# Kernel optimization log

Hardware: AMD Instinct MI355X
Metric: run time of the kernel (lower is better)

The kernel has to match this reference:

```python
import jax, jax.numpy as jnp
import numpy as np

N_NODES = 50000
N_EDGES = 800000
DIM = 128
NUM_GRAPHS = 512


def setup_inputs() -> dict:
    key = jax.random.key(0)
    ks = jax.random.split(key, 12)
    s = 1.0 / np.sqrt(DIM)
    inp = {
        'x': jax.random.normal(ks[0], (N_NODES, DIM), dtype=jnp.float32),
        'edge_index': jax.random.randint(ks[1], (2, N_EDGES), 0, N_NODES, dtype=jnp.int32),
        'batch': jnp.sort(jax.random.randint(ks[2], (N_NODES,), 0, NUM_GRAPHS, dtype=jnp.int32)),
        'W1a': jax.random.uniform(ks[3], (DIM, DIM), jnp.float32, -s, s),
        'b1a': jax.random.uniform(ks[4], (DIM,), jnp.float32, -s, s),
        'W1b': jax.random.uniform(ks[5], (DIM, DIM), jnp.float32, -s, s),
        'b1b': jax.random.uniform(ks[6], (DIM,), jnp.float32, -s, s),
        'W2a': jax.random.uniform(ks[7], (DIM, DIM), jnp.float32, -s, s),
        'b2a': jax.random.uniform(ks[8], (DIM,), jnp.float32, -s, s),
        'W2b': jax.random.uniform(ks[9], (DIM, DIM), jnp.float32, -s, s),
        'b2b': jax.random.uniform(ks[10], (DIM,), jnp.float32, -s, s),
    }
    return inp


def _gin_conv(x, edge_index, Wa, ba, Wb, bb):
    # GINConv with eps=0: h_i = MLP(x_i + sum_{j->i} x_j)
    src, dst = edge_index[0], edge_index[1]
    agg = jax.ops.segment_sum(x[src], dst, num_segments=x.shape[0])  # [N, F]
    h = x + agg
    h = jax.nn.relu(h @ Wa + ba)
    return h @ Wb + bb


def reference(x, edge_index, batch, W1a, b1a, W1b, b1b, W2a, b2a, W2b, b2b):
    h = _gin_conv(x, edge_index, W1a, b1a, W1b, b1b)
    h = _gin_conv(h, edge_index, W2a, b2a, W2b, b2b)
    # global mean pool over graphs
    sums = jax.ops.segment_sum(h, batch, num_segments=NUM_GRAPHS)      # [G, F]
    counts = jax.ops.segment_sum(jnp.ones((h.shape[0],), h.dtype), batch, num_segments=NUM_GRAPHS)
    return sums / jnp.maximum(counts, 1.0)[:, None]
```

## Files before the change

kernel.cpp:

```cpp
#include <hip/hip_runtime.h>

#define DIM 128
#define NBUCK 784
#define EPB 8192
#define ELDS_CAP 2048

typedef unsigned short ushortT;
typedef unsigned int uintT;
typedef _Float16 f16;
typedef __attribute__((ext_vector_type(2))) _Float16 f16x2;
typedef __attribute__((ext_vector_type(8))) _Float16 f16x8;
typedef __attribute__((ext_vector_type(4))) float f32x4;

__device__ inline ushortT f2h(float f) { return __builtin_bit_cast(ushortT, (f16)f); }
__device__ inline float h2f(ushortT s) { return (float)__builtin_bit_cast(f16, s); }

__device__ inline int off_in_row(int k) {
    return (((k >> 5) * 4 + ((k & 15) >> 2)) << 4) + (((k >> 4) & 1) << 3) + ((k & 3) << 1);
}

__device__ inline void add4(f16x2* a, uint4 v) {
    a[0] += __builtin_bit_cast(f16x2, v.x);
    a[1] += __builtin_bit_cast(f16x2, v.y);
    a[2] += __builtin_bit_cast(f16x2, v.z);
    a[3] += __builtin_bit_cast(f16x2, v.w);
}

__device__ inline int wave_iscan(int v) {
    int lane = threadIdx.x & 63;
    #pragma unroll
    for (int d = 1; d < 64; d <<= 1) {
        int t = __shfl_up(v, d, 64);
        if (lane >= d) v += t;
    }
    return v;
}

__global__ __launch_bounds__(256)
void scan_blk_kernel(int* __restrict__ a, int n, int* __restrict__ bsum) {
    __shared__ int ws[4];
    const int tid = threadIdx.x;
    const int i = blockIdx.x * 256 + tid;
    const int lane = tid & 63, wv = tid >> 6;
    int v = (i < n) ? a[i] : 0;
    int isc = wave_iscan(v);
    if (lane == 63) ws[wv] = isc;
    __syncthreads();
    if (tid == 0) { int run = 0; for (int w = 0; w < 4; ++w) { int t = ws[w]; ws[w] = run; run += t; } }
    __syncthreads();
    int e = ws[wv] + isc - v;
    if (i < n) a[i] = e;
    if (tid == 255) bsum[blockIdx.x] = e + v;
}

__global__ __launch_bounds__(256)
void scan_add2_kernel(int* __restrict__ a, int n, const int* __restrict__ bsum) {
    __shared__ int ws[4];
    __shared__ int s_carry;
    const int tid = threadIdx.x;
    int partial = 0;
    for (int i = tid; i < (int)blockIdx.x; i += 256) partial += bsum[i];
    #pragma unroll
    for (int d = 1; d < 64; d <<= 1) partial += __shfl_xor(partial, d, 64);
    if ((tid & 63) == 0) ws[tid >> 6] = partial;
    __syncthreads();
    if (tid == 0) s_carry = ws[0] + ws[1] + ws[2] + ws[3];
    __syncthreads();
    int i = blockIdx.x * 256 + tid;
    if (i < n) a[i] += s_carry;
}

__global__ __launch_bounds__(256)
void histA_kernel(const int* __restrict__ dstIdx, int* __restrict__ histg, int ne, int nblk) {
    __shared__ int h[NBUCK];
    const int j = blockIdx.x;
    for (int i = threadIdx.x; i < NBUCK; i += 256) h[i] = 0;
    __syncthreads();
    const int base = j * EPB;
    const int end = (base + EPB < ne) ? base + EPB : ne;
    for (int i = base + threadIdx.x; i < end; i += 256)
        atomicAdd(&h[dstIdx[i] >> 6], 1);
    __syncthreads();
    for (int b = threadIdx.x; b < NBUCK; b += 256)
        histg[b * nblk + j] = h[b];
}

__global__ __launch_bounds__(256)
void fillA_kernel(const int* __restrict__ srcIdx, const int* __restrict__ dstIdx,
                  const int* __restrict__ Sg, uintT* __restrict__ pairs, int ne, int nblk) {
    __shared__ int cur[NBUCK];
    const int j = blockIdx.x;
    for (int i = threadIdx.x; i < NBUCK; i += 256) cur[i] = Sg[i * nblk + j];
    __syncthreads();
    const int base = j * EPB;
    const int end = (base + EPB < ne) ? base + EPB : ne;
    for (int i = base + threadIdx.x; i < end; i += 256) {
        const int d = dstIdx[i];
        const int s = srcIdx[i];
        const int b = d >> 6;
        const uintT E4 = ((uintT)s << 4) ^ (uintT)(s & 7);
        const int pos = atomicAdd(&cur[b], 1);
        pairs[pos] = (E4 << 6) | (uintT)(d & 63);
    }
}

__global__ __launch_bounds__(256)
void convert_prep_kernel(const float* __restrict__ x, ushortT* __restrict__ xb, int n,
                         const float* __restrict__ W0, const float* __restrict__ W1,
                         const float* __restrict__ W2, const float* __restrict__ W3,
                         ushortT* __restrict__ Wt) {
    if (blockIdx.x < 128) {
        int w = blockIdx.x >> 5;
        const float* W = (w == 0) ? W0 : (w == 1) ? W1 : (w == 2) ? W2 : W3;
        ushortT* dst = Wt + (size_t)w * DIM * DIM;
        int i = (blockIdx.x & 31) * 256 + threadIdx.x;
        int nidx = i >> 6, p = i & 63, k = 2 * p;
        float w0 = W[k * DIM + nidx];
        float w1 = W[(k + 1) * DIM + nidx];
        uintT u = ((uintT)f2h(w1) << 16) | f2h(w0);
        *(uintT*)((char*)dst + (size_t)nidx * 256 + (off_in_row(k) ^ ((nidx & 7) << 4))) = u;
        return;
    }
    int i = (blockIdx.x - 128) * 256 + threadIdx.x;
    int node = i >> 6, p = i & 63;
    if (node >= n) return;
    float2 v = *(const float2*)(x + (size_t)node * DIM + 2 * p);
    uintT u = ((uintT)f2h(v.y) << 16) | f2h(v.x);
    *(uintT*)((char*)xb + (size_t)node * 256 + (off_in_row(2 * p) ^ ((node & 7) << 4))) = u;
}

__global__ __launch_bounds__(128)
void graphoff_zero_kernel(const int* __restrict__ batch, int* __restrict__ goff,
                          float* __restrict__ out, int ng, int nn) {
    const int g = blockIdx.x;
    out[(size_t)g * DIM + threadIdx.x] = 0.0f;
    if (threadIdx.x == 0) {
        int lo = 0, hi = nn;
        while (lo < hi) { int mid = (lo + hi) >> 1; if (batch[mid] < g) lo = mid + 1; else hi = mid; }
        goff[g] = lo;
    }
}

template<int POOL>
__global__ __launch_bounds__(512, 4)
void fused_kernel(const ushortT* __restrict__ Xsrc, ushortT* __restrict__ Yg,
                  const uintT* __restrict__ pairs, const int* __restrict__ Sg, int nblk,
                  const ushortT* __restrict__ WtA, const float* __restrict__ ba,
                  const ushortT* __restrict__ WtB, const float* __restrict__ bb,
                  const int* __restrict__ batch, float* __restrict__ out, int n, int ne) {
    __shared__ __align__(16) ushortT XsU[64 * DIM];
    __shared__ int elds[ELDS_CAP];
    __shared__ int histc[64];
    __shared__ int lstart[65];
    __shared__ int bs[64];

    const int b = blockIdx.x;
    const int node0 = b * 64;
    const int tid = threadIdx.x;
    const int lane = tid & 63, wid = tid >> 6;

    const int base = Sg[b * nblk];
    const int endp = (b + 1 < NBUCK) ? Sg[(b + 1) * nblk] : ne;
    int cnt = endp - base;
    if (cnt > ELDS_CAP) cnt = ELDS_CAP;

    if (tid < 64) {
        histc[tid] = 0;
        if (POOL) { int node = node0 + tid; bs[tid] = (node < n) ? batch[node] : -1; }
    }
    __syncthreads();
    for (int i = tid; i < cnt; i += 512) atomicAdd(&histc[pairs[base + i] & 63], 1);
    __syncthreads();
    if (tid < 64) {
        int v = histc[tid];
        int isc = wave_iscan(v);
        lstart[tid] = isc - v;
        histc[tid] = isc - v;
        if (tid == 63) lstart[64] = isc;
    }
    __syncthreads();
    for (int i = tid; i < cnt; i += 512) {
        uintT p = pairs[base + i];
        int pos = atomicAdd(&histc[p & 63], 1);
        elds[pos] = (int)((p >> 6) << 4);
    }
    __syncthreads();

    const int l15 = lane & 15, g16 = lane >> 4;
    const int lofs = l15 << 4;
    const char* Xc = (const char*)Xsrc;
    for (int t = 0; t < 8; ++t) {
        const int r = wid * 8 + t;
        const int node = node0 + r;
        f16x2 a0[4], a1[4];
        #pragma unroll
        for (int j = 0; j < 4; ++j) { a0[j] = (f16x2)0; a1[j] = (f16x2)0; }
        if (node < n) {
            if (g16 == 0) {
                const int Es = (node << 8) ^ ((node & 7) << 4);
                add4(a0, *(const uint4*)(Xc + (Es ^ lofs)));
            }
            const int s0 = lstart[r], s1 = lstart[r + 1];
            int e = s0;
            for (; e + 16 <= s1; e += 16) {
                const int Ea = elds[e + g16];
                const int Eb = elds[e + 4 + g16];
                const int Ec = elds[e + 8 + g16];
                const int Ed = elds[e + 12 + g16];
                uint4 va = *(const uint4*)(Xc + (Ea ^ lofs));
                uint4 vb = *(const uint4*)(Xc + (Eb ^ lofs));
                uint4 vc = *(const uint4*)(Xc + (Ec ^ lofs));
                uint4 vd = *(const uint4*)(Xc + (Ed ^ lofs));
                add4(a0, va); add4(a1, vb); add4(a0, vc); add4(a1, vd);
            }
            for (; e + 4 <= s1; e += 4) {
                const int E = elds[e + g16];
                add4(a0, *(const uint4*)(Xc + (E ^ lofs)));
            }
            const int rem = s1 - e;
            if (g16 < rem) {
                const int E = elds[e + g16];
                add4(a1, *(const uint4*)(Xc + (E ^ lofs)));
            }
        }
        #pragma unroll
        for (int j = 0; j < 4; ++j) a0[j] += a1[j];
        #pragma unroll
        for (int j = 0; j < 4; ++j) {
            a0[j] += __builtin_bit_cast(f16x2, __shfl_xor(__builtin_bit_cast(int, a0[j]), 16));
            a0[j] += __builtin_bit_cast(f16x2, __shfl_xor(__builtin_bit_cast(int, a0[j]), 32));
        }
        if (lane < 16) {
            uint4 o;
            o.x = __builtin_bit_cast(uintT, a0[0]);
            o.y = __builtin_bit_cast(uintT, a0[1]);
            o.z = __builtin_bit_cast(uintT, a0[2]);
            o.w = __builtin_bit_cast(uintT, a0[3]);
            *(uint4*)((char*)XsU + ((r << 8) ^ (lofs ^ ((r & 7) << 4)))) = o;
        }
    }
    __syncthreads();

    const char* Xl = (const char*)XsU;
    const char* Wa = (const char*)WtA;
    const char* Wb = (const char*)WtB;
    const int g = lane >> 4;
    const int RB = (wid >> 2) * 32, CB = (wid & 3) * 32;

    f32x4 acc2[2][2];
    #pragma unroll
    for (int nt = 0; nt < 2; ++nt) {
        float bv = ba[CB + nt * 16 + l15];
        #pragma unroll
        for (int mt = 0; mt < 2; ++mt) acc2[mt][nt] = (f32x4){bv, bv, bv, bv};
    }
    #pragma unroll
    for (int ks = 0; ks < 4; ++ks) {
        const int cb = (ks * 4 + g) << 4;
        f16x8 a0, a1, bf[2];
        { int r0 = RB + l15, r1 = RB + 16 + l15;
          a0 = *(const f16x8*)(Xl + r0 * 256 + (cb ^ ((r0 & 7) << 4)));
          a1 = *(const f16x8*)(Xl + r1 * 256 + (cb ^ ((r1 & 7) << 4))); }
        #pragma unroll
        for (int nt = 0; nt < 2; ++nt) {
            int rn = CB + nt * 16 + l15;
            bf[nt] = *(const f16x8*)(Wa + rn * 256 + (cb ^ ((rn & 7) << 4)));
        }
        #pragma unroll
        for (int nt = 0; nt < 2; ++nt) {
            acc2[0][nt] = __builtin_amdgcn_mfma_f32_16x16x32_f16(a0, bf[nt], acc2[0][nt], 0, 0, 0);
            acc2[1][nt] = __builtin_amdgcn_mfma_f32_16x16x32_f16(a1, bf[nt], acc2[1][nt], 0, 0, 0);
        }
    }
    #pragma unroll
    for (int mt = 0; mt < 2; ++mt)
        #pragma unroll
        for (int nt = 0; nt < 2; ++nt)
            #pragma unroll
            for (int c = 0; c < 4; ++c) acc2[mt][nt][c] = fmaxf(acc2[mt][nt][c], 0.0f);

    __syncthreads();

    #pragma unroll
    for (int nt = 0; nt < 2; ++nt) {
        const int k = CB + nt * 16 + l15;
        const int offk = off_in_row(k);
        #pragma unroll
        for (int mt = 0; mt < 2; ++mt)
            #pragma unroll
            for (int r = 0; r < 4; ++r) {
                int row = RB + mt * 16 + 4 * g + r;
                *(ushortT*)((char*)XsU + row * 256 + (offk ^ ((row & 7) << 4))) = f2h(acc2[mt][nt][r]);
            }
    }
    __syncthreads();

    #pragma unroll
    for (int nt = 0; nt < 2; ++nt) {
        float bv = bb[CB + nt * 16 + l15];
        #pragma unroll
        for (int mt = 0; mt < 2; ++mt) acc2[mt][nt] = (f32x4){bv, bv, bv, bv};
    }
    #pragma unroll
    for (int ks = 0; ks < 4; ++ks) {
        const int cb = (ks * 4 + g) << 4;
        f16x8 a0, a1, bf[2];
        { int r0 = RB + l15, r1 = RB + 16 + l15;
          a0 = *(const f16x8*)(Xl + r0 * 256 + (cb ^ ((r0 & 7) << 4)));
          a1 = *(const f16x8*)(Xl + r1 * 256 + (cb ^ ((r1 & 7) << 4))); }
        #pragma unroll
        for (int nt = 0; nt < 2; ++nt) {
            int rn = CB + nt * 16 + l15;
            bf[nt] = *(const f16x8*)(Wb + rn * 256 + (cb ^ ((rn & 7) << 4)));
        }
        #pragma unroll
        for (int nt = 0; nt < 2; ++nt) {
            acc2[0][nt] = __builtin_amdgcn_mfma_f32_16x16x32_f16(a0, bf[nt], acc2[0][nt], 0, 0, 0);
            acc2[1][nt] = __builtin_amdgcn_mfma_f32_16x16x32_f16(a1, bf[nt], acc2[1][nt], 0, 0, 0);
        }
    }

    if (POOL) {
        __syncthreads();
        #pragma unroll
        for (int nt = 0; nt < 2; ++nt) {
            const int k = CB + nt * 16 + l15;
            const int offk = off_in_row(k);
            #pragma unroll
            for (int mt = 0; mt < 2; ++mt)
                #pragma unroll
                for (int r = 0; r < 4; ++r) {
                    int row = RB + mt * 16 + 4 * g + r;
                    *(ushortT*)((char*)XsU + row * 256 + (offk ^ ((row & 7) << 4))) = f2h(acc2[mt][nt][r]);
                }
        }
        __syncthreads();
        const int col = tid & 127, rh = tid >> 7;
        const int offc = off_in_row(col);
        const int r0 = rh * 16, r1 = r0 + 16;
        float run = 0.0f;
        int gcur = bs[r0];
        for (int r = r0; r < r1; ++r) {
            int gb = bs[r];
            if (gb != gcur) {
                if (gcur >= 0) atomicAdd(&out[(size_t)gcur * DIM + col], run);
                run = 0.0f; gcur = gb;
            }
            run += h2f(*(const ushortT*)((const char*)XsU + r * 256 + (offc ^ ((r & 7) << 4))));
        }
        if (gcur >= 0) atomicAdd(&out[(size_t)gcur * DIM + col], run);
    } else {
        #pragma unroll
        for (int nt = 0; nt < 2; ++nt) {
            const int k = CB + nt * 16 + l15;
            const int offk = off_in_row(k);
            #pragma unroll
            for (int mt = 0; mt < 2; ++mt)
                #pragma unroll
                for (int r = 0; r < 4; ++r) {
                    int row = RB + mt * 16 + 4 * g + r;
                    int node = node0 + row;
                    if (node < n)
                        *(ushortT*)((char*)Yg + (size_t)node * 256 + (offk ^ ((row & 7) << 4))) = f2h(acc2[mt][nt][r]);
                }
        }
    }
}

__global__ __launch_bounds__(256)
void divide_kernel(float* __restrict__ out, const int* __restrict__ goff, int ng, int nn) {
    int i = blockIdx.x * 256 + threadIdx.x;
    if (i >= ng * DIM) return;
    int gidx = i >> 7;
    int cnt = ((gidx + 1 < ng) ? goff[gidx + 1] : nn) - goff[gidx];
    out[i] /= fmaxf((float)cnt, 1.0f);
}

extern "C" void kernel_launch(void* const* d_in, const int* in_sizes, int n_in,
                              void* d_out, int out_size, void* d_ws, size_t ws_size,
                              hipStream_t stream) {
    const float* x     = (const float*)d_in[0];
    const int*   ei    = (const int*)d_in[1];
    const int*   batch = (const int*)d_in[2];
    const float* W1a = (const float*)d_in[3];
    const float* b1a = (const float*)d_in[4];
    const float* W1b = (const float*)d_in[5];
    const float* b1b = (const float*)d_in[6];
    const float* W2a = (const float*)d_in[7];
    const float* b2a = (const float*)d_in[8];
    const float* W2b = (const float*)d_in[9];
    const float* b2b = (const float*)d_in[10];
    float* out = (float*)d_out;

    const int NN = in_sizes[0] / DIM;
    const int NE = in_sizes[1] / 2;
    const int NG = out_size / DIM;
    const int NN2 = (NN + 63) & ~63;
    const int nblk = (NE + EPB - 1) / EPB;
    const int nS = NBUCK * nblk;
    const int nScanBlk = (nS + 255) / 256;

    ushortT* xb    = (ushortT*)d_ws;
    ushortT* bufB  = xb   + (size_t)NN2 * DIM;
    ushortT* wt    = bufB + (size_t)NN2 * DIM;
    uintT*   pairs = (uintT*)(wt + 4 * DIM * DIM);
    int*     Sg    = (int*)(pairs + (size_t)NE);
    int*     bsum  = Sg + nS;
    int*     goff  = bsum + nScanBlk;

    const int* srcIdx = ei;
    const int* dstIdx = ei + NE;

    histA_kernel<<<nblk, 256, 0, stream>>>(dstIdx, Sg, NE, nblk);
    scan_blk_kernel<<<nScanBlk, 256, 0, stream>>>(Sg, nS, bsum);
    scan_add2_kernel<<<nScanBlk, 256, 0, stream>>>(Sg, nS, bsum);
    fillA_kernel<<<nblk, 256, 0, stream>>>(srcIdx, dstIdx, Sg, pairs, NE, nblk);

    convert_prep_kernel<<<128 + (NN * 64) / 256, 256, 0, stream>>>(x, xb, NN, W1a, W1b, W2a, W2b, wt);
    graphoff_zero_kernel<<<NG, 128, 0, stream>>>(batch, goff, out, NG, NN);

    fused_kernel<0><<<NBUCK, 512, 0, stream>>>(xb, bufB, pairs, Sg, nblk,
                                               wt, b1a, wt + DIM * DIM, b1b,
                                               batch, out, NN, NE);
    fused_kernel<1><<<NBUCK, 512, 0, stream>>>(bufB, (ushortT*)nullptr, pairs, Sg, nblk,
                                               wt + 2 * DIM * DIM, b2a, wt + 3 * DIM * DIM, b2b,
                                               batch, out, NN, NE);

    divide_kernel<<<(out_size + 255) / 256, 256, 0, stream>>>(out, goff, NG, NN);
}
```

Baseline: 130.5 us.

## Merge prep kernels and widen fused GIN kernel to 1024 threads per node row

Merges the histogram, weight/feature conversion and graph-offset/zeroing kernels into one launch, which removes launch gaps. Each fused block now runs 1024 threads (16 waves). In the gather phase each 16-lane group owns one node and walks its edges serially, so the cross-group shuffle reduction is gone. The MFMA tiles shrink to 16 rows per wave, giving more waves to hide gather latency. The trade-off is less ILP per lane in the gather loop and more register pressure per CU.

Measured after the change: 136.1 us. 4.3% more time.

```diff
diff --git a/kernel.cpp b/kernel.cpp
--- a/kernel.cpp
+++ b/kernel.cpp
@@ -71,18 +71,59 @@
 }
 
 __global__ __launch_bounds__(256)
-void histA_kernel(const int* __restrict__ dstIdx, int* __restrict__ histg, int ne, int nblk) {
+void prep_kernel(const int* __restrict__ dstIdx, int* __restrict__ histg, int ne, int nblk,
+                 const float* __restrict__ x, ushortT* __restrict__ xb, int n, int nxconv,
+                 const float* __restrict__ W0, const float* __restrict__ W1,
+                 const float* __restrict__ W2, const float* __restrict__ W3,
+                 ushortT* __restrict__ Wt,
+                 const int* __restrict__ batch, int* __restrict__ goff,
+                 float* __restrict__ out, int ng) {
     __shared__ int h[NBUCK];
-    const int j = blockIdx.x;
-    for (int i = threadIdx.x; i < NBUCK; i += 256) h[i] = 0;
-    __syncthreads();
-    const int base = j * EPB;
-    const int end = (base + EPB < ne) ? base + EPB : ne;
-    for (int i = base + threadIdx.x; i < end; i += 256)
-        atomicAdd(&h[dstIdx[i] >> 6], 1);
-    __syncthreads();
-    for (int b = threadIdx.x; b < NBUCK; b += 256)
-        histg[b * nblk + j] = h[b];
+    const int bid = blockIdx.x;
+    const int tid = threadIdx.x;
+    if (bid < nblk) {
+        for (int i = tid; i < NBUCK; i += 256) h[i] = 0;
+        __syncthreads();
+        const int base = bid * EPB;
+        const int end = (base + EPB < ne) ? base + EPB : ne;
+        for (int i = base + tid; i < end; i += 256)
+            atomicAdd(&h[dstIdx[i] >> 6], 1);
+        __syncthreads();
+        for (int b = tid; b < NBUCK; b += 256)
+            histg[b * nblk + bid] = h[b];
+        return;
+    }
+    if (bid < nblk + 128) {
+        int r = bid - nblk;
+        int w = r >> 5;
+        const float* W = (w == 0) ? W0 : (w == 1) ? W1 : (w == 2) ? W2 : W3;
+        ushortT* dst = Wt + (size_t)w * DIM * DIM;
+        int i = (r & 31) * 256 + tid;
+        int nidx = i >> 6, p = i & 63, k = 2 * p;
+        float w0 = W[k * DIM + nidx];
+        float w1 = W[(k + 1) * DIM + nidx];
+        uintT u = ((uintT)f2h(w1) << 16) | f2h(w0);
+        *(uintT*)((char*)dst + (size_t)nidx * 256 + (off_in_row(k) ^ ((nidx & 7) << 4))) = u;
+        return;
+    }
+    if (bid < nblk + 128 + nxconv) {
+        int i = (bid - nblk - 128) * 256 + tid;
+        int node = i >> 6, p = i & 63;
+        if (node >= n) return;
+        float2 v = *(const float2*)(x + (size_t)node * DIM + 2 * p);
+        uintT u = ((uintT)f2h(v.y) << 16) | f2h(v.x);
+        *(uintT*)((char*)xb + (size_t)node * 256 + (off_in_row(2 * p) ^ ((node & 7) << 4))) = u;
+        return;
+    }
+    const int g = bid - nblk - 128 - nxconv;
+    if (g < ng) {
+        if (tid < 128) out[(size_t)g * DIM + tid] = 0.0f;
+        if (tid == 128) {
+            int lo = 0, hi = n;
+            while (lo < hi) { int mid = (lo + hi) >> 1; if (batch[mid] < g) lo = mid + 1; else hi = mid; }
+            goff[g] = lo;
+        }
+    }
 }
 
 __global__ __launch_bounds__(256)
@@ -104,45 +145,8 @@
     }
 }
 
-__global__ __launch_bounds__(256)
-void convert_prep_kernel(const float* __restrict__ x, ushortT* __restrict__ xb, int n,
-                         const float* __restrict__ W0, const float* __restrict__ W1,
-                         const float* __restrict__ W2, const float* __restrict__ W3,
-                         ushortT* __restrict__ Wt) {
-    if (blockIdx.x < 128) {
-        int w = blockIdx.x >> 5;
-        const float* W = (w == 0) ? W0 : (w == 1) ? W1 : (w == 2) ? W2 : W3;
-        ushortT* dst = Wt + (size_t)w * DIM * DIM;
-        int i = (blockIdx.x & 31) * 256 + threadIdx.x;
-        int nidx = i >> 6, p = i & 63, k = 2 * p;
-        float w0 = W[k * DIM + nidx];
-        float w1 = W[(k + 1) * DIM + nidx];
-        uintT u = ((uintT)f2h(w1) << 16) | f2h(w0);
-        *(uintT*)((char*)dst + (size_t)nidx * 256 + (off_in_row(k) ^ ((nidx & 7) << 4))) = u;
-        return;
-    }
-    int i = (blockIdx.x - 128) * 256 + threadIdx.x;
-    int node = i >> 6, p = i & 63;
-    if (node >= n) return;
-    float2 v = *(const float2*)(x + (size_t)node * DIM + 2 * p);
-    uintT u = ((uintT)f2h(v.y) << 16) | f2h(v.x);
-    *(uintT*)((char*)xb + (size_t)node * 256 + (off_in_row(2 * p) ^ ((node & 7) << 4))) = u;
-}
-
-__global__ __launch_bounds__(128)
-void graphoff_zero_kernel(const int* __restrict__ batch, int* __restrict__ goff,
-                          float* __restrict__ out, int ng, int nn) {
-    const int g = blockIdx.x;
-    out[(size_t)g * DIM + threadIdx.x] = 0.0f;
-    if (threadIdx.x == 0) {
-        int lo = 0, hi = nn;
-        while (lo < hi) { int mid = (lo + hi) >> 1; if (batch[mid] < g) lo = mid + 1; else hi = mid; }
-        goff[g] = lo;
-    }
-}
-
 template<int POOL>
-__global__ __launch_bounds__(512, 4)
+__global__ __launch_bounds__(1024, 2)
 void fused_kernel(const ushortT* __restrict__ Xsrc, ushortT* __restrict__ Yg,
                   const uintT* __restrict__ pairs, const int* __restrict__ Sg, int nblk,
                   const ushortT* __restrict__ WtA, const float* __restrict__ ba,
@@ -169,7 +173,7 @@
         if (POOL) { int node = node0 + tid; bs[tid] = (node < n) ? batch[node] : -1; }
     }
     __syncthreads();
-    for (int i = tid; i < cnt; i += 512) atomicAdd(&histc[pairs[base + i] & 63], 1);
+    for (int i = tid; i < cnt; i += 1024) atomicAdd(&histc[pairs[base + i] & 63], 1);
     __syncthreads();
     if (tid < 64) {
         int v = histc[tid];
@@ -179,7 +183,7 @@
         if (tid == 63) lstart[64] = isc;
     }
     __syncthreads();
-    for (int i = tid; i < cnt; i += 512) {
+    for (int i = tid; i < cnt; i += 1024) {
         uintT p = pairs[base + i];
         int pos = atomicAdd(&histc[p & 63], 1);
         elds[pos] = (int)((p >> 6) << 4);
@@ -189,55 +193,34 @@
     const int l15 = lane & 15, g16 = lane >> 4;
     const int lofs = l15 << 4;
     const char* Xc = (const char*)Xsrc;
-    for (int t = 0; t < 8; ++t) {
-        const int r = wid * 8 + t;
+    {
+        const int r = (wid << 2) + g16;
         const int node = node0 + r;
         f16x2 a0[4], a1[4];
         #pragma unroll
         for (int j = 0; j < 4; ++j) { a0[j] = (f16x2)0; a1[j] = (f16x2)0; }
         if (node < n) {
-            if (g16 == 0) {
-                const int Es = (node << 8) ^ ((node & 7) << 4);
-                add4(a0, *(const uint4*)(Xc + (Es ^ lofs)));
-            }
+            const int Es = (node << 8) ^ ((node & 7) << 4);
+            add4(a0, *(const uint4*)(Xc + (Es ^ lofs)));
             const int s0 = lstart[r], s1 = lstart[r + 1];
             int e = s0;
-            for (; e + 16 <= s1; e += 16) {
-                const int Ea = elds[e + g16];
-                const int Eb = elds[e + 4 + g16];
-                const int Ec = elds[e + 8 + g16];
-                const int Ed = elds[e + 12 + g16];
+            for (; e + 2 <= s1; e += 2) {
+                const int Ea = elds[e];
+                const int Eb = elds[e + 1];
                 uint4 va = *(const uint4*)(Xc + (Ea ^ lofs));
                 uint4 vb = *(const uint4*)(Xc + (Eb ^ lofs));
-                uint4 vc = *(const uint4*)(Xc + (Ec ^ lofs));
-                uint4 vd = *(const uint4*)(Xc + (Ed ^ lofs));
-                add4(a0, va); add4(a1, vb); add4(a0, vc); add4(a1, vd);
+                add4(a0, va); add4(a1, vb);
             }
-            for (; e + 4 <= s1; e += 4) {
-                const int E = elds[e + g16];
-                add4(a0, *(const uint4*)(Xc + (E ^ lofs)));
-            }
-            const int rem = s1 - e;
-            if (g16 < rem) {
-                const int E = elds[e + g16];
-                add4(a1, *(const uint4*)(Xc + (E ^ lofs)));
-            }
+            if (e < s1) add4(a0, *(const uint4*)(Xc + (elds[e] ^ lofs)));
         }
         #pragma unroll
         for (int j = 0; j < 4; ++j) a0[j] += a1[j];
-        #pragma unroll
-        for (int j = 0; j < 4; ++j) {
-            a0[j] += __builtin_bit_cast(f16x2, __shfl_xor(__builtin_bit_cast(int, a0[j]), 16));
-            a0[j] += __builtin_bit_cast(f16x2, __shfl_xor(__builtin_bit_cast(int, a0[j]), 32));
-        }
-        if (lane < 16) {
-            uint4 o;
-            o.x = __builtin_bit_cast(uintT, a0[0]);
-            o.y = __builtin_bit_cast(uintT, a0[1]);
-            o.z = __builtin_bit_cast(uintT, a0[2]);
-            o.w = __builtin_bit_cast(uintT, a0[3]);
-            *(uint4*)((char*)XsU + ((r << 8) ^ (lofs ^ ((r & 7) << 4)))) = o;
-        }
+        uint4 o;
+        o.x = __builtin_bit_cast(uintT, a0[0]);
+        o.y = __builtin_bit_cast(uintT, a0[1]);
+        o.z = __builtin_bit_cast(uintT, a0[2]);
+        o.w = __builtin_bit_cast(uintT, a0[3]);
+        *(uint4*)((char*)XsU + ((r << 8) ^ (lofs ^ ((r & 7) << 4)))) = o;
     }
     __syncthreads();
 
@@ -245,39 +228,33 @@
     const char* Wa = (const char*)WtA;
     const char* Wb = (const char*)WtB;
     const int g = lane >> 4;
-    const int RB = (wid >> 2) * 32, CB = (wid & 3) * 32;
-
-    f32x4 acc2[2][2];
+    const int RB = (wid >> 2) * 16, CB = (wid & 3) * 32;
+
+    f32x4 acc2[2];
     #pragma unroll
     for (int nt = 0; nt < 2; ++nt) {
         float bv = ba[CB + nt * 16 + l15];
-        #pragma unroll
-        for (int mt = 0; mt < 2; ++mt) acc2[mt][nt] = (f32x4){bv, bv, bv, bv};
+        acc2[nt] = (f32x4){bv, bv, bv, bv};
     }
     #pragma unroll
     for (int ks = 0; ks < 4; ++ks) {
         const int cb = (ks * 4 + g) << 4;
-        f16x8 a0, a1, bf[2];
-        { int r0 = RB + l15, r1 = RB + 16 + l15;
-          a0 = *(const f16x8*)(Xl + r0 * 256 + (cb ^ ((r0 & 7) << 4)));
-          a1 = *(const f16x8*)(Xl + r1 * 256 + (cb ^ ((r1 & 7) << 4))); }
+        f16x8 a0, bf[2];
+        { int r0 = RB + l15;
+          a0 = *(const f16x8*)(Xl + r0 * 256 + (cb ^ ((r0 & 7) << 4))); }
         #pragma unroll
         for (int nt = 0; nt < 2; ++nt) {
             int rn = CB + nt * 16 + l15;
             bf[nt] = *(const f16x8*)(Wa + rn * 256 + (cb ^ ((rn & 7) << 4)));
         }
         #pragma unroll
-        for (int nt = 0; nt < 2; ++nt) {
-            acc2[0][nt] = __builtin_amdgcn_mfma_f32_16x16x32_f16(a0, bf[nt], acc2[0][nt], 0, 0, 0);
-            acc2[1][nt] = __builtin_amdgcn_mfma_f32_16x16x32_f16(a1, bf[nt], acc2[1][nt], 0, 0, 0);
-        }
-    }
-    #pragma unroll
-    for (int mt = 0; mt < 2; ++mt)
-        #pragma unroll
         for (int nt = 0; nt < 2; ++nt)
-            #pragma unroll
-            for (int c = 0; c < 4; ++c) acc2[mt][nt][c] = fmaxf(acc2[mt][nt][c], 0.0f);
+            acc2[nt] = __builtin_amdgcn_mfma_f32_16x16x32_f16(a0, bf[nt], acc2[nt], 0, 0, 0);
+    }
+    #pragma unroll
+    for (int nt = 0; nt < 2; ++nt)
+        #pragma unroll
+        for (int c = 0; c < 4; ++c) acc2[nt][c] = fmaxf(acc2[nt][c], 0.0f);
 
     __syncthreads();
 
@@ -286,38 +263,32 @@
         const int k = CB + nt * 16 + l15;
         const int offk = off_in_row(k);
         #pragma unroll
-        for (int mt = 0; mt < 2; ++mt)
-            #pragma unroll
-            for (int r = 0; r < 4; ++r) {
-                int row = RB + mt * 16 + 4 * g + r;
-                *(ushortT*)((char*)XsU + row * 256 + (offk ^ ((row & 7) << 4))) = f2h(acc2[mt][nt][r]);
-            }
+        for (int r = 0; r < 4; ++r) {
+            int row = RB + 4 * g + r;
+            *(ushortT*)((char*)XsU + row * 256 + (offk ^ ((row & 7) << 4))) = f2h(acc2[nt][r]);
+        }
     }
     __syncthreads();
 
     #pragma unroll
     for (int nt = 0; nt < 2; ++nt) {
         float bv = bb[CB + nt * 16 + l15];
-        #pragma unroll
-        for (int mt = 0; mt < 2; ++mt) acc2[mt][nt] = (f32x4){bv, bv, bv, bv};
+        acc2[nt] = (f32x4){bv, bv, bv, bv};
     }
     #pragma unroll
     for (int ks = 0; ks < 4; ++ks) {
         const int cb = (ks * 4 + g) << 4;
-        f16x8 a0, a1, bf[2];
-        { int r0 = RB + l15, r1 = RB + 16 + l15;
-          a0 = *(const f16x8*)(Xl + r0 * 256 + (cb ^ ((r0 & 7) << 4)));
-          a1 = *(const f16x8*)(Xl + r1 * 256 + (cb ^ ((r1 & 7) << 4))); }
+        f16x8 a0, bf[2];
+        { int r0 = RB + l15;
+          a0 = *(const f16x8*)(Xl + r0 * 256 + (cb ^ ((r0 & 7) << 4))); }
         #pragma unroll
         for (int nt = 0; nt < 2; ++nt) {
             int rn = CB + nt * 16 + l15;
             bf[nt] = *(const f16x8*)(Wb + rn * 256 + (cb ^ ((rn & 7) << 4)));
         }
         #pragma unroll
-        for (int nt = 0; nt < 2; ++nt) {
-            acc2[0][nt] = __builtin_amdgcn_mfma_f32_16x16x32_f16(a0, bf[nt], acc2[0][nt], 0, 0, 0);
-            acc2[1][nt] = __builtin_amdgcn_mfma_f32_16x16x32_f16(a1, bf[nt], acc2[1][nt], 0, 0, 0);
-        }
+        for (int nt = 0; nt < 2; ++nt)
+            acc2[nt] = __builtin_amdgcn_mfma_f32_16x16x32_f16(a0, bf[nt], acc2[nt], 0, 0, 0);
     }
 
     if (POOL) {
@@ -327,17 +298,15 @@
             const int k = CB + nt * 16 + l15;
             const int offk = off_in_row(k);
             #pragma unroll
-            for (int mt = 0; mt < 2; ++mt)
-                #pragma unroll
-                for (int r = 0; r < 4; ++r) {
-                    int row = RB + mt * 16 + 4 * g + r;
-                    *(ushortT*)((char*)XsU + row * 256 + (offk ^ ((row & 7) << 4))) = f2h(acc2[mt][nt][r]);
-                }
+            for (int r = 0; r < 4; ++r) {
+                int row = RB + 4 * g + r;
+                *(ushortT*)((char*)XsU + row * 256 + (offk ^ ((row & 7) << 4))) = f2h(acc2[nt][r]);
+            }
         }
         __syncthreads();
         const int col = tid & 127, rh = tid >> 7;
         const int offc = off_in_row(col);
-        const int r0 = rh * 16, r1 = r0 + 16;
+        const int r0 = rh * 8, r1 = r0 + 8;
         float run = 0.0f;
         int gcur = bs[r0];
         for (int r = r0; r < r1; ++r) {
@@ -355,14 +324,12 @@
             const int k = CB + nt * 16 + l15;
             const int offk = off_in_row(k);
             #pragma unroll
-            for (int mt = 0; mt < 2; ++mt)
-                #pragma unroll
-                for (int r = 0; r < 4; ++r) {
-                    int row = RB + mt * 16 + 4 * g + r;
-                    int node = node0 + row;
-                    if (node < n)
-                        *(ushortT*)((char*)Yg + (size_t)node * 256 + (offk ^ ((row & 7) << 4))) = f2h(acc2[mt][nt][r]);
-                }
+            for (int r = 0; r < 4; ++r) {
+                int row = RB + 4 * g + r;
+                int node = node0 + row;
+                if (node < n)
+                    *(ushortT*)((char*)Yg + (size_t)node * 256 + (offk ^ ((row & 7) << 4))) = f2h(acc2[nt][r]);
+            }
         }
     }
 }
@@ -399,6 +366,7 @@
     const int nblk = (NE + EPB - 1) / EPB;
     const int nS = NBUCK * nblk;
     const int nScanBlk = (nS + 255) / 256;
+    const int nxconv = (NN * 64 + 255) / 256;
 
     ushortT* xb    = (ushortT*)d_ws;
     ushortT* bufB  = xb   + (size_t)NN2 * DIM;
@@ -411,20 +379,20 @@
     const int* srcIdx = ei;
     const int* dstIdx = ei + NE;
 
-    histA_kernel<<<nblk, 256, 0, stream>>>(dstIdx, Sg, NE, nblk);
+    prep_kernel<<<nblk + 128 + nxconv + NG, 256, 0, stream>>>(
+        dstIdx, Sg, NE, nblk, x, xb, NN, nxconv,
+        W1a, W1b, W2a, W2b, wt, batch, goff, out, NG);
+
     scan_blk_kernel<<<nScanBlk, 256, 0, stream>>>(Sg, nS, bsum);
     scan_add2_kernel<<<nScanBlk, 256, 0, stream>>>(Sg, nS, bsum);
     fillA_kernel<<<nblk, 256, 0, stream>>>(srcIdx, dstIdx, Sg, pairs, NE, nblk);
 
-    convert_prep_kernel<<<128 + (NN * 64) / 256, 256, 0, stream>>>(x, xb, NN, W1a, W1b, W2a, W2b, wt);
-    graphoff_zero_kernel<<<NG, 128, 0, stream>>>(batch, goff, out, NG, NN);
-
-    fused_kernel<0><<<NBUCK, 512, 0, stream>>>(xb, bufB, pairs, Sg, nblk,
-                                               wt, b1a, wt + DIM * DIM, b1b,
-                                               batch, out, NN, NE);
-    fused_kernel<1><<<NBUCK, 512, 0, stream>>>(bufB, (ushortT*)nullptr, pairs, Sg, nblk,
-                                               wt + 2 * DIM * DIM, b2a, wt + 3 * DIM * DIM, b2b,
-                                               batch, out, NN, NE);
+    fused_kernel<0><<<NBUCK, 1024, 0, stream>>>(xb, bufB, pairs, Sg, nblk,
+                                                wt, b1a, wt + DIM * DIM, b1b,
+                                                batch, out, NN, NE);
+    fused_kernel<1><<<NBUCK, 1024, 0, stream>>>(bufB, (ushortT*)nullptr, pairs, Sg, nblk,
+                                                wt + 2 * DIM * DIM, b2a, wt + 3 * DIM * DIM, b2b,
+                                                batch, out, NN, NE);
 
     divide_kernel<<<(out_size + 255) / 256, 256, 0, stream>>>(out, goff, NG, NN);
 }
```

## Merge prep kernels into one launch and precompute per-bucket CSR once

Applied to the files above, without the earlier changes.

The histogram, weight/feature conversion and graph-offset/zeroing kernels are merged into a single launch, which removes two kernel launches. A new sortB kernel does the per-bucket local sort once and writes a CSR array plus per-node offsets. Both fused GIN layers then just copy the CSR into LDS instead of each rerunning the histogram, scan and atomic scatter. This adds one kernel launch and an extra global write and read of the CSR array.

Measured after the change: 124.5 us. -4.6%, faster.

```diff
diff --git a/kernel.cpp b/kernel.cpp
--- a/kernel.cpp
+++ b/kernel.cpp
@@ -71,18 +71,59 @@
 }
 
 __global__ __launch_bounds__(256)
-void histA_kernel(const int* __restrict__ dstIdx, int* __restrict__ histg, int ne, int nblk) {
+void prep_kernel(const int* __restrict__ dstIdx, int* __restrict__ histg, int ne, int nblk,
+                 const float* __restrict__ x, ushortT* __restrict__ xb, int n, int nxconv,
+                 const float* __restrict__ W0, const float* __restrict__ W1,
+                 const float* __restrict__ W2, const float* __restrict__ W3,
+                 ushortT* __restrict__ Wt,
+                 const int* __restrict__ batch, int* __restrict__ goff,
+                 float* __restrict__ out, int ng) {
     __shared__ int h[NBUCK];
-    const int j = blockIdx.x;
-    for (int i = threadIdx.x; i < NBUCK; i += 256) h[i] = 0;
-    __syncthreads();
-    const int base = j * EPB;
-    const int end = (base + EPB < ne) ? base + EPB : ne;
-    for (int i = base + threadIdx.x; i < end; i += 256)
-        atomicAdd(&h[dstIdx[i] >> 6], 1);
-    __syncthreads();
-    for (int b = threadIdx.x; b < NBUCK; b += 256)
-        histg[b * nblk + j] = h[b];
+    const int bid = blockIdx.x;
+    const int tid = threadIdx.x;
+    if (bid < nblk) {
+        for (int i = tid; i < NBUCK; i += 256) h[i] = 0;
+        __syncthreads();
+        const int base = bid * EPB;
+        const int end = (base + EPB < ne) ? base + EPB : ne;
+        for (int i = base + tid; i < end; i += 256)
+            atomicAdd(&h[dstIdx[i] >> 6], 1);
+        __syncthreads();
+        for (int b = tid; b < NBUCK; b += 256)
+            histg[b * nblk + bid] = h[b];
+        return;
+    }
+    if (bid < nblk + 128) {
+        int r = bid - nblk;
+        int w = r >> 5;
+        const float* W = (w == 0) ? W0 : (w == 1) ? W1 : (w == 2) ? W2 : W3;
+        ushortT* dst = Wt + (size_t)w * DIM * DIM;
+        int i = (r & 31) * 256 + tid;
+        int nidx = i >> 6, p = i & 63, k = 2 * p;
+        float w0 = W[k * DIM + nidx];
+        float w1 = W[(k + 1) * DIM + nidx];
+        uintT u = ((uintT)f2h(w1) << 16) | f2h(w0);
+        *(uintT*)((char*)dst + (size_t)nidx * 256 + (off_in_row(k) ^ ((nidx & 7) << 4))) = u;
+        return;
+    }
+    if (bid < nblk + 128 + nxconv) {
+        int i = (bid - nblk - 128) * 256 + tid;
+        int node = i >> 6, p = i & 63;
+        if (node >= n) return;
+        float2 v = *(const float2*)(x + (size_t)node * DIM + 2 * p);
+        uintT u = ((uintT)f2h(v.y) << 16) | f2h(v.x);
+        *(uintT*)((char*)xb + (size_t)node * 256 + (off_in_row(2 * p) ^ ((node & 7) << 4))) = u;
+        return;
+    }
+    const int g = bid - nblk - 128 - nxconv;
+    if (g < ng) {
+        if (tid < 128) out[(size_t)g * DIM + tid] = 0.0f;
+        if (tid == 128) {
+            int lo = 0, hi = n;
+            while (lo < hi) { int mid = (lo + hi) >> 1; if (batch[mid] < g) lo = mid + 1; else hi = mid; }
+            goff[g] = lo;
+        }
+    }
 }
 
 __global__ __launch_bounds__(256)
@@ -105,52 +146,50 @@
 }
 
 __global__ __launch_bounds__(256)
-void convert_prep_kernel(const float* __restrict__ x, ushortT* __restrict__ xb, int n,
-                         const float* __restrict__ W0, const float* __restrict__ W1,
-                         const float* __restrict__ W2, const float* __restrict__ W3,
-                         ushortT* __restrict__ Wt) {
-    if (blockIdx.x < 128) {
-        int w = blockIdx.x >> 5;
-        const float* W = (w == 0) ? W0 : (w == 1) ? W1 : (w == 2) ? W2 : W3;
-        ushortT* dst = Wt + (size_t)w * DIM * DIM;
-        int i = (blockIdx.x & 31) * 256 + threadIdx.x;
-        int nidx = i >> 6, p = i & 63, k = 2 * p;
-        float w0 = W[k * DIM + nidx];
-        float w1 = W[(k + 1) * DIM + nidx];
-        uintT u = ((uintT)f2h(w1) << 16) | f2h(w0);
-        *(uintT*)((char*)dst + (size_t)nidx * 256 + (off_in_row(k) ^ ((nidx & 7) << 4))) = u;
-        return;
-    }
-    int i = (blockIdx.x - 128) * 256 + threadIdx.x;
-    int node = i >> 6, p = i & 63;
-    if (node >= n) return;
-    float2 v = *(const float2*)(x + (size_t)node * DIM + 2 * p);
-    uintT u = ((uintT)f2h(v.y) << 16) | f2h(v.x);
-    *(uintT*)((char*)xb + (size_t)node * 256 + (off_in_row(2 * p) ^ ((node & 7) << 4))) = u;
-}
-
-__global__ __launch_bounds__(128)
-void graphoff_zero_kernel(const int* __restrict__ batch, int* __restrict__ goff,
-                          float* __restrict__ out, int ng, int nn) {
-    const int g = blockIdx.x;
-    out[(size_t)g * DIM + threadIdx.x] = 0.0f;
-    if (threadIdx.x == 0) {
-        int lo = 0, hi = nn;
-        while (lo < hi) { int mid = (lo + hi) >> 1; if (batch[mid] < g) lo = mid + 1; else hi = mid; }
-        goff[g] = lo;
+void sortB_kernel(const uintT* __restrict__ pairs, const int* __restrict__ Sg,
+                  int* __restrict__ off, int* __restrict__ csr, int ne, int nn, int nblk) {
+    __shared__ int hist[64];
+    __shared__ int cur[64];
+    __shared__ uintT plds[ELDS_CAP];
+    const int b = blockIdx.x;
+    const int tid = threadIdx.x;
+    const int base = Sg[b * nblk];
+    const int endp = (b + 1 < NBUCK) ? Sg[(b + 1) * nblk] : ne;
+    int cnt = endp - base;
+    if (cnt > ELDS_CAP) cnt = ELDS_CAP;
+    if (tid < 64) hist[tid] = 0;
+    __syncthreads();
+    for (int i = tid; i < cnt; i += 256) {
+        uintT p = pairs[base + i];
+        plds[i] = p;
+        atomicAdd(&hist[p & 63], 1);
+    }
+    __syncthreads();
+    if (tid < 64) {
+        int v = hist[tid];
+        int isc = wave_iscan(v);
+        cur[tid] = base + isc - v;
+        int node = b * 64 + tid;
+        if (node < nn) off[node] = base + isc;
+    }
+    __syncthreads();
+    for (int i = tid; i < cnt; i += 256) {
+        uintT p = plds[i];
+        int pos = atomicAdd(&cur[p & 63], 1);
+        csr[pos] = (int)((p >> 6) << 4);
     }
 }
 
 template<int POOL>
 __global__ __launch_bounds__(512, 4)
 void fused_kernel(const ushortT* __restrict__ Xsrc, ushortT* __restrict__ Yg,
-                  const uintT* __restrict__ pairs, const int* __restrict__ Sg, int nblk,
+                  const int* __restrict__ csr, const int* __restrict__ offg,
+                  const int* __restrict__ Sg, int nblk,
                   const ushortT* __restrict__ WtA, const float* __restrict__ ba,
                   const ushortT* __restrict__ WtB, const float* __restrict__ bb,
                   const int* __restrict__ batch, float* __restrict__ out, int n, int ne) {
     __shared__ __align__(16) ushortT XsU[64 * DIM];
     __shared__ int elds[ELDS_CAP];
-    __shared__ int histc[64];
     __shared__ int lstart[65];
     __shared__ int bs[64];
 
@@ -164,25 +203,13 @@
     int cnt = endp - base;
     if (cnt > ELDS_CAP) cnt = ELDS_CAP;
 
+    for (int i = tid; i < cnt; i += 512) elds[i] = csr[base + i];
     if (tid < 64) {
-        histc[tid] = 0;
-        if (POOL) { int node = node0 + tid; bs[tid] = (node < n) ? batch[node] : -1; }
-    }
-    __syncthreads();
-    for (int i = tid; i < cnt; i += 512) atomicAdd(&histc[pairs[base + i] & 63], 1);
-    __syncthreads();
-    if (tid < 64) {
-        int v = histc[tid];
-        int isc = wave_iscan(v);
-        lstart[tid] = isc - v;
-        histc[tid] = isc - v;
-        if (tid == 63) lstart[64] = isc;
-    }
-    __syncthreads();
-    for (int i = tid; i < cnt; i += 512) {
-        uintT p = pairs[base + i];
-        int pos = atomicAdd(&histc[p & 63], 1);
-        elds[pos] = (int)((p >> 6) << 4);
+        int node = node0 + tid;
+        int v = (node < n) ? (offg[node] - base) : cnt;
+        lstart[tid + 1] = (v > cnt) ? cnt : v;
+        if (tid == 0) lstart[0] = 0;
+        if (POOL) bs[tid] = (node < n) ? batch[node] : -1;
     }
     __syncthreads();
 
@@ -399,30 +426,34 @@
     const int nblk = (NE + EPB - 1) / EPB;
     const int nS = NBUCK * nblk;
     const int nScanBlk = (nS + 255) / 256;
+    const int nxconv = (NN * 64 + 255) / 256;
 
     ushortT* xb    = (ushortT*)d_ws;
     ushortT* bufB  = xb   + (size_t)NN2 * DIM;
     ushortT* wt    = bufB + (size_t)NN2 * DIM;
     uintT*   pairs = (uintT*)(wt + 4 * DIM * DIM);
-    int*     Sg    = (int*)(pairs + (size_t)NE);
+    int*     csr   = (int*)(pairs + (size_t)NE);
+    int*     Sg    = csr + NE;
     int*     bsum  = Sg + nS;
     int*     goff  = bsum + nScanBlk;
+    int*     off   = goff + NG;
 
     const int* srcIdx = ei;
     const int* dstIdx = ei + NE;
 
-    histA_kernel<<<nblk, 256, 0, stream>>>(dstIdx, Sg, NE, nblk);
+    prep_kernel<<<nblk + 128 + nxconv + NG, 256, 0, stream>>>(
+        dstIdx, Sg, NE, nblk, x, xb, NN, nxconv,
+        W1a, W1b, W2a, W2b, wt, batch, goff, out, NG);
+
     scan_blk_kernel<<<nScanBlk, 256, 0, stream>>>(Sg, nS, bsum);
     scan_add2_kernel<<<nScanBlk, 256, 0, stream>>>(Sg, nS, bsum);
     fillA_kernel<<<nblk, 256, 0, stream>>>(srcIdx, dstIdx, Sg, pairs, NE, nblk);
-
-    convert_prep_kernel<<<128 + (NN * 64) / 256, 256, 0, stream>>>(x, xb, NN, W1a, W1b, W2a, W2b, wt);
-    graphoff_zero_kernel<<<NG, 128, 0, stream>>>(batch, goff, out, NG, NN);
-
-    fused_kernel<0><<<NBUCK, 512, 0, stream>>>(xb, bufB, pairs, Sg, nblk,
+    sortB_kernel<<<NBUCK, 256, 0, stream>>>(pairs, Sg, off, csr, NE, NN, nblk);
+
+    fused_kernel<0><<<NBUCK, 512, 0, stream>>>(xb, bufB, csr, off, Sg, nblk,
                                                wt, b1a, wt + DIM * DIM, b1b,
                                                batch, out, NN, NE);
-    fused_kernel<1><<<NBUCK, 512, 0, stream>>>(bufB, (ushortT*)nullptr, pairs, Sg, nblk,
+    fused_kernel<1><<<NBUCK, 512, 0, stream>>>(bufB, (ushortT*)nullptr, csr, off, Sg, nblk,
                                                wt + 2 * DIM * DIM, b2a, wt + 3 * DIM * DIM, b2b,
                                                batch, out, NN, NE);
 
```
